# Performance work log

Hardware: AMD Instinct MI355X
Metric: run time of the kernel (lower is better)

## Reference

```python
import jax, jax.numpy as jnp
import numpy as np

B, S, H = 2, 1024, 1024
NH, NKV, HD = 16, 4, 64
E, K, I = 8, 2, 3584
EPS = 1e-5
THETA = 1e6


def setup_inputs() -> dict:
    key = jax.random.key(0)
    ks = jax.random.split(key, 12)
    sc = 0.02
    return {
        "hidden_states": jax.random.normal(ks[0], (B, S, H), jnp.float32),
        "ln1_w": jnp.ones((H,), jnp.float32),
        "wq": jax.random.normal(ks[1], (H, NH * HD), jnp.float32) * sc,
        "wk": jax.random.normal(ks[2], (H, NKV * HD), jnp.float32) * sc,
        "wv": jax.random.normal(ks[3], (H, NKV * HD), jnp.float32) * sc,
        "wo": jax.random.normal(ks[4], (NH * HD, H), jnp.float32) * sc,
        "ln2_w": jnp.ones((H,), jnp.float32),
        "router_w": jax.random.normal(ks[5], (H, E), jnp.float32) * sc,
        "w_gate": jax.random.normal(ks[6], (E, H, I), jnp.float32) * sc,
        "w_up": jax.random.normal(ks[7], (E, H, I), jnp.float32) * sc,
        "w_down": jax.random.normal(ks[8], (E, I, H), jnp.float32) * sc,
    }


def _rmsnorm(x, w):
    xf = x.astype(jnp.float32)
    return (xf * jax.lax.rsqrt(jnp.mean(xf * xf, axis=-1, keepdims=True) + EPS)).astype(x.dtype) * w


def _rope_cos_sin():
    inv_freq = 1.0 / (THETA ** (jnp.arange(0, HD, 2, dtype=jnp.float32) / HD))
    ang = jnp.arange(S, dtype=jnp.float32)[:, None] * inv_freq[None, :]  # [S, HD//2]
    emb = jnp.concatenate([ang, ang], axis=-1)  # [S, HD]
    return jnp.cos(emb)[None, :, None, :], jnp.sin(emb)[None, :, None, :]


def _rotate_half(x):
    return jnp.concatenate([-x[..., HD // 2:], x[..., : HD // 2]], axis=-1)


def _attention(x, wq, wk, wv, wo):
    q = (x @ wq).reshape(B, S, NH, HD)
    k = (x @ wk).reshape(B, S, NKV, HD)
    v = (x @ wv).reshape(B, S, NKV, HD)
    cos, sin = _rope_cos_sin()
    q = q * cos + _rotate_half(q) * sin
    k = k * cos + _rotate_half(k) * sin
    rep = NH // NKV
    k = jnp.repeat(k, rep, axis=2)  # [B,S,NH,HD]
    v = jnp.repeat(v, rep, axis=2)
    scores = jnp.einsum("bqhd,bkhd->bhqk", q, k) / jnp.sqrt(jnp.float32(HD))
    causal = jnp.tril(jnp.ones((S, S), bool))
    scores = jnp.where(causal[None, None], scores, jnp.float32(-1e9))
    probs = jax.nn.softmax(scores, axis=-1)
    out = jnp.einsum("bhqk,bkhd->bqhd", probs, v).reshape(B, S, NH * HD)
    return out @ wo


def _moe(x, router_w, w_gate, w_up, w_down):
    t = x.reshape(B * S, H)  # [T,H]
    logits = t @ router_w  # [T,E]
    probs = jax.nn.softmax(logits.astype(jnp.float32), axis=-1)
    top_v, top_i = jax.lax.top_k(probs, K)
    top_v = top_v / jnp.sum(top_v, axis=-1, keepdims=True)  # normalize_top_k_affinities
    # dense combine weights [T,E]
    dense_w = jnp.sum(jax.nn.one_hot(top_i, E, dtype=t.dtype) * top_v[..., None], axis=1)
    out = jnp.zeros_like(t)
    for e in range(E):  # small fixed expert loop (E=8)
        g = jax.nn.silu(t @ w_gate[e]) * (t @ w_up[e])
        out = out + dense_w[:, e:e + 1] * (g @ w_down[e])
    return out.reshape(B, S, H)


def reference(hidden_states, ln1_w, wq, wk, wv, wo, ln2_w, router_w, w_gate, w_up, w_down):
    residual = hidden_states
    h = _rmsnorm(hidden_states, ln1_w)
    h = residual + _attention(h, wq, wk, wv, wo)
    residual = h
    h2 = _rmsnorm(h, ln2_w)
    h = residual + _moe(h2, router_w, w_gate, w_up, w_down)
    return h
```

## Files before the change

### kernel.cpp

```cpp
#include <hip/hip_runtime.h>
#include <hip/hip_bf16.h>
#include <math.h>

#define B_ 2
#define S_ 1024
#define H_ 1024
#define NH_ 16
#define NKV_ 4
#define HD_ 64
#define E_ 8
#define I_ 3584
#define T_ (B_*S_)

#define BM 64
#define BN 64
#define MBM 128
#define DBM 64
#define MBK 64

typedef __bf16 bf16x8 __attribute__((ext_vector_type(8)));
typedef float f32x4 __attribute__((ext_vector_type(4)));

__device__ __forceinline__ __bf16 bf_hi(float f) { return (__bf16)f; }
__device__ __forceinline__ __bf16 bf_lo(float f, __bf16 h) { return (__bf16)(f - (float)h); }

__device__ __forceinline__ int swz128(int row, int col) {
    return (row * 128 + col * 2) ^ ((row & 7) << 4);
}

__global__ __launch_bounds__(256) void split_bf16_kernel(
    const float* __restrict__ src, __bf16* __restrict__ hi, __bf16* __restrict__ lo,
    float scale, int n8)
{
    int idx = blockIdx.x * 256 + threadIdx.x;
    if (idx >= n8) return;
    const float4* s = (const float4*)src + (size_t)idx * 2;
    float4 a = s[0], b = s[1];
    float f[8] = {a.x, a.y, a.z, a.w, b.x, b.y, b.z, b.w};
    bf16x8 vh, vl;
#pragma unroll
    for (int i = 0; i < 8; i++) {
        float x = f[i] * scale;
        __bf16 h = bf_hi(x);
        vh[i] = h;
        vl[i] = bf_lo(x, h);
    }
    ((bf16x8*)hi)[idx] = vh;
    ((bf16x8*)lo)[idx] = vl;
}

__global__ __launch_bounds__(256) void transpose_cvt_kernel(
    const float* __restrict__ src, __bf16* __restrict__ dst, int M, int N)
{
    int e = blockIdx.z;
    src += (size_t)e * M * N;
    dst += (size_t)e * M * N;
    int n0 = blockIdx.x * 64, m0 = blockIdx.y * 64;
    __shared__ __bf16 Ts[64][72];
    int tid = threadIdx.x;
#pragma unroll
    for (int i = 0; i < 16; i++) {
        int row = i * 4 + (tid >> 6);
        int col = tid & 63;
        Ts[row][col] = (__bf16)src[(size_t)(m0 + row) * N + n0 + col];
    }
    __syncthreads();
#pragma unroll
    for (int j = 0; j < 2; j++) {
        int n = (tid >> 3) + j * 32;
        int k8 = (tid & 7) * 8;
        bf16x8 v;
#pragma unroll
        for (int ii = 0; ii < 8; ii++) v[ii] = Ts[k8 + ii][n];
        *(bf16x8*)(dst + (size_t)(n0 + n) * M + m0 + k8) = v;
    }
}

__global__ __launch_bounds__(256) void rmsnorm_kernel(
    const float* __restrict__ x, const float* __restrict__ w,
    __bf16* __restrict__ outb, float* __restrict__ outf)
{
    int row = blockIdx.x;
    int tid = threadIdx.x;
    const float* xr = x + (size_t)row * H_;
    float vals[4];
    float ss = 0.f;
#pragma unroll
    for (int i = 0; i < 4; i++) {
        vals[i] = xr[tid + 256 * i];
        ss += vals[i] * vals[i];
    }
#pragma unroll
    for (int off = 32; off; off >>= 1) ss += __shfl_xor(ss, off);
    __shared__ float red[4];
    int wid = tid >> 6;
    if ((tid & 63) == 0) red[wid] = ss;
    __syncthreads();
    float tot = red[0] + red[1] + red[2] + red[3];
    float scale = rsqrtf(tot * (1.0f / H_) + 1e-5f);
#pragma unroll
    for (int i = 0; i < 4; i++) {
        float y = vals[i] * scale * w[tid + 256 * i];
        outb[(size_t)row * H_ + tid + 256 * i] = (__bf16)y;
        if (outf) outf[(size_t)row * H_ + tid + 256 * i] = y;
    }
}

__global__ __launch_bounds__(256) void gemm_bf16bt(
    const __bf16* __restrict__ A, const __bf16* __restrict__ BT,
    float* __restrict__ C, const float* __restrict__ res,
    int M, int N, int Kd)
{
    int m0 = blockIdx.y * DBM;
    int n0 = blockIdx.x * BN;
    __shared__ __bf16 As[2][DBM * MBK];
    __shared__ __bf16 Bs[2][BN * MBK];
    int tid = threadIdx.x;
    int lane = tid & 63, wid = tid >> 6;
    f32x4 acc[4] = {};
    int ar = tid >> 2, ac = (tid & 3) * 16;
    int bn = tid >> 2, bc = (tid & 3) * 16;
    const __bf16* abase = A + (size_t)(m0 + ar) * Kd + ac;
    const __bf16* bbase = BT + (size_t)(n0 + bn) * Kd + bc;
    {
        char* Asb = (char*)As[0];
        char* Bsb = (char*)Bs[0];
#pragma unroll
        for (int g = 0; g < 2; g++) {
            *(bf16x8*)(Asb + swz128(ar, ac + g * 8)) = *(const bf16x8*)(abase + g * 8);
            *(bf16x8*)(Bsb + swz128(bn, bc + g * 8)) = *(const bf16x8*)(bbase + g * 8);
        }
    }
    bf16x8 pa[2], pb[2];
    if (Kd > MBK) {
#pragma unroll
        for (int g = 0; g < 2; g++) {
            pa[g] = *(const bf16x8*)(abase + MBK + g * 8);
            pb[g] = *(const bf16x8*)(bbase + MBK + g * 8);
        }
    }
    int cur = 0;
    int r = lane & 15, q8 = (lane >> 4) * 8;
    for (int kt = 0; kt < Kd; kt += MBK) {
        __syncthreads();
        char* Asb = (char*)As[cur];
        char* Bsb = (char*)Bs[cur];
#pragma unroll
        for (int kk = 0; kk < 2; kk++) {
            bf16x8 af = *(const bf16x8*)(Asb + swz128(wid * 16 + r, kk * 32 + q8));
            bf16x8 bfr[4];
#pragma unroll
            for (int n = 0; n < 4; n++)
                bfr[n] = *(const bf16x8*)(Bsb + swz128(n * 16 + r, kk * 32 + q8));
#pragma unroll
            for (int n = 0; n < 4; n++)
                acc[n] = __builtin_amdgcn_mfma_f32_16x16x32_bf16(af, bfr[n], acc[n], 0, 0, 0);
        }
        int kn = kt + MBK;
        if (kn < Kd) {
            char* Asw = (char*)As[cur ^ 1];
            char* Bsw = (char*)Bs[cur ^ 1];
#pragma unroll
            for (int g = 0; g < 2; g++) {
                *(bf16x8*)(Asw + swz128(ar, ac + g * 8)) = pa[g];
                *(bf16x8*)(Bsw + swz128(bn, bc + g * 8)) = pb[g];
            }
            int k2 = kn + MBK;
            if (k2 < Kd) {
#pragma unroll
                for (int g = 0; g < 2; g++) {
                    pa[g] = *(const bf16x8*)(abase + k2 + g * 8);
                    pb[g] = *(const bf16x8*)(bbase + k2 + g * 8);
                }
            }
            cur ^= 1;
        }
    }
    int cl = lane & 15, rb = (lane >> 4) * 4;
#pragma unroll
    for (int n = 0; n < 4; n++)
#pragma unroll
        for (int j = 0; j < 4; j++) {
            int row = m0 + wid * 16 + rb + j;
            int col = n0 + n * 16 + cl;
            size_t o = (size_t)row * N + col;
            float v = acc[n][j];
            if (res) v += res[o];
            C[o] = v;
        }
}

__global__ void rope_split_kernel(
    const float* __restrict__ x, __bf16* __restrict__ hi, __bf16* __restrict__ lo,
    float scale, int heads, int total)
{
    int idx = blockIdx.x * blockDim.x + threadIdx.x;
    if (idx >= total) return;
    int j = idx & 31;
    int th = idx >> 5;
    int h = th % heads;
    int t = th / heads;
    int s = t & (S_ - 1);
    float inv = powf(1e6f, -(float)j / 32.0f);
    float ang = (float)s * inv;
    float c = cosf(ang), sn = sinf(ang);
    size_t base = (size_t)t * heads * HD_ + (size_t)h * HD_;
    float x1 = x[base + j], x2 = x[base + 32 + j];
    float y1 = (x1 * c - x2 * sn) * scale;
    float y2 = (x2 * c + x1 * sn) * scale;
    __bf16 h1 = bf_hi(y1), h2 = bf_hi(y2);
    hi[base + j] = h1;       lo[base + j] = bf_lo(y1, h1);
    hi[base + 32 + j] = h2;  lo[base + 32 + j] = bf_lo(y2, h2);
}

#define LP 72
__global__ __launch_bounds__(256) void flash_kernel(
    const __bf16* __restrict__ qhi, const __bf16* __restrict__ qlo_g,
    const __bf16* __restrict__ khi, const __bf16* __restrict__ klo,
    const __bf16* __restrict__ vhi, const __bf16* __restrict__ vlo,
    __bf16* __restrict__ o)
{
    __shared__ __bf16 Ks [64][LP];
    __shared__ __bf16 Ksl[64][LP];
    __shared__ __bf16 Vt [64][LP];
    __shared__ __bf16 Vtl[64][LP];
    __shared__ __bf16 Pl [4][16][LP];
    __shared__ __bf16 Pll[4][16][LP];

    int tid = threadIdx.x;
    int lane = tid & 63, wid = tid >> 6;
    int qr = lane & 15, quad = lane >> 4;
    int qt = (S_ / 16 - 1) - blockIdx.x;
    int kvh = blockIdx.y, b = blockIdx.z;
    int h = kvh * 4 + wid;
    int s0 = qt * 16;

    size_t qoff = ((size_t)(b * S_ + s0 + qr) * NH_ + h) * HD_ + quad * 8;
    bf16x8 qf[2], qlo[2];
#pragma unroll
    for (int ks = 0; ks < 2; ks++) {
        qf[ks]  = *(const bf16x8*)(qhi  + qoff + ks * 32);
        qlo[ks] = *(const bf16x8*)(qlo_g + qoff + ks * 32);
    }

    float m_run[4], l_run[4];
    f32x4 o_acc[4] = {};
#pragma unroll
    for (int j = 0; j < 4; j++) { m_run[j] = -1e30f; l_run[j] = 0.f; }

    int skey = tid >> 2, shd0 = (tid & 3) * 16;
    int vhd = tid & 63, vkey0 = (tid >> 6) * 16;

    for (int kt = 0; kt <= s0 + 15; kt += 64) {
        __syncthreads();
        {
            size_t koff = ((size_t)(b * S_ + kt + skey) * NKV_ + kvh) * HD_ + shd0;
            *(bf16x8*)&Ks [skey][shd0]     = *(const bf16x8*)(khi + koff);
            *(bf16x8*)&Ks [skey][shd0 + 8] = *(const bf16x8*)(khi + koff + 8);
            *(bf16x8*)&Ksl[skey][shd0]     = *(const bf16x8*)(klo + koff);
            *(bf16x8*)&Ksl[skey][shd0 + 8] = *(const bf16x8*)(klo + koff + 8);
        }
        {
            const __bf16* vh = vhi + ((size_t)(b * S_ + kt + vkey0) * NKV_ + kvh) * HD_ + vhd;
            const __bf16* vl = vlo + ((size_t)(b * S_ + kt + vkey0) * NKV_ + kvh) * HD_ + vhd;
            bf16x8 th0, th1, tl0, tl1;
#pragma unroll
            for (int i = 0; i < 8; i++) {
                th0[i] = vh[(size_t)i * (NKV_ * HD_)];
                th1[i] = vh[(size_t)(i + 8) * (NKV_ * HD_)];
                tl0[i] = vl[(size_t)i * (NKV_ * HD_)];
                tl1[i] = vl[(size_t)(i + 8) * (NKV_ * HD_)];
            }
            *(bf16x8*)&Vt [vhd][vkey0]     = th0;
            *(bf16x8*)&Vt [vhd][vkey0 + 8] = th1;
            *(bf16x8*)&Vtl[vhd][vkey0]     = tl0;
            *(bf16x8*)&Vtl[vhd][vkey0 + 8] = tl1;
        }
        __syncthreads();

        f32x4 sc4[4];
#pragma unroll
        for (int sub = 0; sub < 4; sub++) {
            int krow = sub * 16 + qr;
            bf16x8 kh0 = *(const bf16x8*)&Ks [krow][quad * 8];
            bf16x8 kh1 = *(const bf16x8*)&Ks [krow][32 + quad * 8];
            bf16x8 kl0 = *(const bf16x8*)&Ksl[krow][quad * 8];
            bf16x8 kl1 = *(const bf16x8*)&Ksl[krow][32 + quad * 8];
            f32x4 z = {};
            z = __builtin_amdgcn_mfma_f32_16x16x32_bf16(qf[0],  kh0, z, 0, 0, 0);
            z = __builtin_amdgcn_mfma_f32_16x16x32_bf16(qf[1],  kh1, z, 0, 0, 0);
            z = __builtin_amdgcn_mfma_f32_16x16x32_bf16(qlo[0], kh0, z, 0, 0, 0);
            z = __builtin_amdgcn_mfma_f32_16x16x32_bf16(qlo[1], kh1, z, 0, 0, 0);
            z = __builtin_amdgcn_mfma_f32_16x16x32_bf16(qf[0],  kl0, z, 0, 0, 0);
            z = __builtin_amdgcn_mfma_f32_16x16x32_bf16(qf[1],  kl1, z, 0, 0, 0);
            sc4[sub] = z;
        }
        if (kt + 63 > s0) {
#pragma unroll
            for (int sub = 0; sub < 4; sub++)
#pragma unroll
                for (int j = 0; j < 4; j++) {
                    int key = kt + sub * 16 + qr;
                    int row = s0 + quad * 4 + j;
                    if (key > row) sc4[sub][j] = -1e30f;
                }
        }
#pragma unroll
        for (int j = 0; j < 4; j++) {
            float mx = fmaxf(fmaxf(sc4[0][j], sc4[1][j]), fmaxf(sc4[2][j], sc4[3][j]));
#pragma unroll
            for (int off = 1; off < 16; off <<= 1) mx = fmaxf(mx, __shfl_xor(mx, off));
            float mn = fmaxf(m_run[j], mx);
            float scale = __expf(m_run[j] - mn);
            m_run[j] = mn;
            float rs = 0.f;
#pragma unroll
            for (int sub = 0; sub < 4; sub++) {
                float pe = __expf(sc4[sub][j] - mn);
                sc4[sub][j] = pe;
                rs += pe;
            }
#pragma unroll
            for (int off = 1; off < 16; off <<= 1) rs += __shfl_xor(rs, off);
            l_run[j] = l_run[j] * scale + rs;
#pragma unroll
            for (int sub = 0; sub < 4; sub++) o_acc[sub][j] *= scale;
        }
#pragma unroll
        for (int sub = 0; sub < 4; sub++)
#pragma unroll
            for (int j = 0; j < 4; j++) {
                float pe = sc4[sub][j];
                __bf16 hh = bf_hi(pe);
                Pl [wid][quad * 4 + j][sub * 16 + qr] = hh;
                Pll[wid][quad * 4 + j][sub * 16 + qr] = bf_lo(pe, hh);
            }
        __syncthreads();
        bf16x8 ph0 = *(const bf16x8*)&Pl [wid][qr][quad * 8];
        bf16x8 ph1 = *(const bf16x8*)&Pl [wid][qr][32 + quad * 8];
        bf16x8 pl0 = *(const bf16x8*)&Pll[wid][qr][quad * 8];
        bf16x8 pl1 = *(const bf16x8*)&Pll[wid][qr][32 + quad * 8];
#pragma unroll
        for (int sub = 0; sub < 4; sub++) {
            int vrow = sub * 16 + qr;
            bf16x8 vh0 = *(const bf16x8*)&Vt [vrow][quad * 8];
            bf16x8 vh1 = *(const bf16x8*)&Vt [vrow][32 + quad * 8];
            bf16x8 vl0 = *(const bf16x8*)&Vtl[vrow][quad * 8];
            bf16x8 vl1 = *(const bf16x8*)&Vtl[vrow][32 + quad * 8];
            o_acc[sub] = __builtin_amdgcn_mfma_f32_16x16x32_bf16(ph0, vh0, o_acc[sub], 0, 0, 0);
            o_acc[sub] = __builtin_amdgcn_mfma_f32_16x16x32_bf16(ph1, vh1, o_acc[sub], 0, 0, 0);
            o_acc[sub] = __builtin_amdgcn_mfma_f32_16x16x32_bf16(ph0, vl0, o_acc[sub], 0, 0, 0);
            o_acc[sub] = __builtin_amdgcn_mfma_f32_16x16x32_bf16(ph1, vl1, o_acc[sub], 0, 0, 0);
            o_acc[sub] = __builtin_amdgcn_mfma_f32_16x16x32_bf16(pl0, vh0, o_acc[sub], 0, 0, 0);
            o_acc[sub] = __builtin_amdgcn_mfma_f32_16x16x32_bf16(pl1, vh1, o_acc[sub], 0, 0, 0);
        }
    }
#pragma unroll
    for (int j = 0; j < 4; j++) {
        float inv = 1.f / l_run[j];
        int row = s0 + quad * 4 + j;
#pragma unroll
        for (int sub = 0; sub < 4; sub++)
            o[((size_t)(b * S_ + row) * NH_ + h) * HD_ + sub * 16 + qr] = (__bf16)(o_acc[sub][j] * inv);
    }
}

__global__ __launch_bounds__(256) void router_kernel(
    const float* __restrict__ xn, const float* __restrict__ rw,
    int* __restrict__ top_i, float* __restrict__ top_w)
{
    int wid = threadIdx.x >> 6, lane = threadIdx.x & 63;
    int t = blockIdx.x * 4 + wid;
    const float* xr = xn + (size_t)t * H_;
    float acc[E_] = {};
    for (int c = 0; c < H_ / 64; c++) {
        float xd = xr[c * 64 + lane];
        const float* wrow = rw + (size_t)(c * 64 + lane) * E_;
#pragma unroll
        for (int e = 0; e < E_; e++) acc[e] += xd * wrow[e];
    }
#pragma unroll
    for (int e = 0; e < E_; e++) {
        float r = acc[e];
#pragma unroll
        for (int off = 32; off; off >>= 1) r += __shfl_xor(r, off);
        acc[e] = r;
    }
    if (lane == 0) {
        float mx = acc[0];
        for (int e = 1; e < E_; e++) mx = fmaxf(mx, acc[e]);
        float p[E_], sum = 0.f;
        for (int e = 0; e < E_; e++) { p[e] = __expf(acc[e] - mx); sum += p[e]; }
        float inv_s = 1.f / sum;
        for (int e = 0; e < E_; e++) p[e] *= inv_s;
        int i0 = 0;
        for (int e = 1; e < E_; e++) if (p[e] > p[i0]) i0 = e;
        int i1 = (i0 == 0) ? 1 : 0;
        for (int e = 0; e < E_; e++) if (e != i0 && p[e] > p[i1]) i1 = e;
        float v0 = p[i0], v1 = p[i1], inv = 1.f / (v0 + v1);
        top_i[t * 2] = i0; top_i[t * 2 + 1] = i1;
        top_w[t * 2] = v0 * inv; top_w[t * 2 + 1] = v1 * inv;
    }
}

__global__ void assign_kernel(
    const int* __restrict__ top_i, const float* __restrict__ top_w,
    int* __restrict__ tlist, int* __restrict__ pair_pos,
    int* __restrict__ counts, int* __restrict__ offsets)
{
    __shared__ int cnt[E_], off[E_], fill[E_];
    int tid = threadIdx.x;
    if (tid < E_) { cnt[tid] = 0; fill[tid] = 0; }
    __syncthreads();
    for (int t = tid; t < T_; t += 256) {
        atomicAdd(&cnt[top_i[t * 2]], 1);
        atomicAdd(&cnt[top_i[t * 2 + 1]], 1);
    }
    __syncthreads();
    if (tid == 0) {
        int o = 0;
        for (int e = 0; e < E_; e++) { off[e] = o; o += cnt[e]; }
    }
    __syncthreads();
    for (int t = tid; t < T_; t += 256) {
        for (int j = 0; j < 2; j++) {
            int e = top_i[t * 2 + j];
            int pos = off[e] + atomicAdd(&fill[e], 1);
            tlist[pos] = t;
            pair_pos[t * 2 + j] = pos;
        }
    }
    __syncthreads();
    if (tid < E_) { counts[tid] = cnt[tid]; offsets[tid] = off[tid]; }
}

__global__ __launch_bounds__(256) void moe_gemm_gateup(
    const __bf16* __restrict__ Xb, const __bf16* __restrict__ WgT, const __bf16* __restrict__ WuT,
    __bf16* __restrict__ act, const int* __restrict__ tlist,
    const int* __restrict__ counts, const int* __restrict__ offsets)
{
    int e = blockIdx.z;
    int cnt = counts[e], off = offsets[e];
    int m0 = blockIdx.y * MBM;
    if (m0 >= cnt) return;
    int n0 = blockIdx.x * BN;
    const __bf16* Bg = WgT + (size_t)e * H_ * I_;
    const __bf16* Bu = WuT + (size_t)e * H_ * I_;
    __shared__ __bf16 As[2][MBM * MBK];
    __shared__ __bf16 Gs[2][BN * MBK];
    __shared__ __bf16 Us[2][BN * MBK];
    __shared__ int rowidx[MBM];
    int tid = threadIdx.x;
    if (tid < MBM) {
        int rl = m0 + tid;
        rowidx[tid] = tlist[off + ((rl < cnt) ? rl : 0)];
    }
    __syncthreads();
    int lane = tid & 63, wid = tid >> 6;
    f32x4 accg[2][4] = {}, accu[2][4] = {};
    int ar = tid >> 1, ac = (tid & 1) * 32;
    int bn = tid >> 2, bc = (tid & 3) * 16;
    const __bf16* abase = Xb + (size_t)rowidx[ar] * H_ + ac;
    const __bf16* gbase = Bg + (size_t)(n0 + bn) * H_ + bc;
    const __bf16* ubase = Bu + (size_t)(n0 + bn) * H_ + bc;
    {
        char* Asb = (char*)As[0];
        char* Gsb = (char*)Gs[0];
        char* Usb = (char*)Us[0];
#pragma unroll
        for (int g = 0; g < 4; g++)
            *(bf16x8*)(Asb + swz128(ar, ac + g * 8)) = *(const bf16x8*)(abase + g * 8);
#pragma unroll
        for (int g = 0; g < 2; g++) {
            *(bf16x8*)(Gsb + swz128(bn, bc + g * 8)) = *(const bf16x8*)(gbase + g * 8);
            *(bf16x8*)(Usb + swz128(bn, bc + g * 8)) = *(const bf16x8*)(ubase + g * 8);
        }
    }
    bf16x8 pa[4], pg[2], pu[2];
    if (H_ > MBK) {
#pragma unroll
        for (int g = 0; g < 4; g++) pa[g] = *(const bf16x8*)(abase + MBK + g * 8);
#pragma unroll
        for (int g = 0; g < 2; g++) {
            pg[g] = *(const bf16x8*)(gbase + MBK + g * 8);
            pu[g] = *(const bf16x8*)(ubase + MBK + g * 8);
        }
    }
    int cur = 0;
    int r = lane & 15, q8 = (lane >> 4) * 8;
    for (int kt = 0; kt < H_; kt += MBK) {
        __syncthreads();
        char* Asb = (char*)As[cur];
        char* Gsb = (char*)Gs[cur];
        char* Usb = (char*)Us[cur];
#pragma unroll
        for (int kk = 0; kk < 2; kk++) {
            bf16x8 af[2], gf[4], uf[4];
#pragma unroll
            for (int m = 0; m < 2; m++)
                af[m] = *(const bf16x8*)(Asb + swz128(wid * 32 + m * 16 + r, kk * 32 + q8));
#pragma unroll
            for (int n = 0; n < 4; n++) {
                gf[n] = *(const bf16x8*)(Gsb + swz128(n * 16 + r, kk * 32 + q8));
                uf[n] = *(const bf16x8*)(Usb + swz128(n * 16 + r, kk * 32 + q8));
            }
#pragma unroll
            for (int m = 0; m < 2; m++)
#pragma unroll
                for (int n = 0; n < 4; n++) {
                    accg[m][n] = __builtin_amdgcn_mfma_f32_16x16x32_bf16(af[m], gf[n], accg[m][n], 0, 0, 0);
                    accu[m][n] = __builtin_amdgcn_mfma_f32_16x16x32_bf16(af[m], uf[n], accu[m][n], 0, 0, 0);
                }
        }
        int kn = kt + MBK;
        if (kn < H_) {
            char* Asw = (char*)As[cur ^ 1];
            char* Gsw = (char*)Gs[cur ^ 1];
            char* Usw = (char*)Us[cur ^ 1];
#pragma unroll
            for (int g = 0; g < 4; g++) *(bf16x8*)(Asw + swz128(ar, ac + g * 8)) = pa[g];
#pragma unroll
            for (int g = 0; g < 2; g++) {
                *(bf16x8*)(Gsw + swz128(bn, bc + g * 8)) = pg[g];
                *(bf16x8*)(Usw + swz128(bn, bc + g * 8)) = pu[g];
            }
            int k2 = kn + MBK;
            if (k2 < H_) {
#pragma unroll
                for (int g = 0; g < 4; g++) pa[g] = *(const bf16x8*)(abase + k2 + g * 8);
#pragma unroll
                for (int g = 0; g < 2; g++) {
                    pg[g] = *(const bf16x8*)(gbase + k2 + g * 8);
                    pu[g] = *(const bf16x8*)(ubase + k2 + g * 8);
                }
            }
            cur ^= 1;
        }
    }
    int cl = lane & 15, rb = (lane >> 4) * 4;
#pragma unroll
    for (int m = 0; m < 2; m++)
#pragma unroll
        for (int n = 0; n < 4; n++)
#pragma unroll
            for (int j = 0; j < 4; j++) {
                int rl = m0 + wid * 32 + m * 16 + rb + j;
                if (rl >= cnt) continue;
                int col = n0 + n * 16 + cl;
                float g = accg[m][n][j], u = accu[m][n][j];
                float sig = 1.f / (1.f + __expf(-g));
                act[(size_t)(off + rl) * I_ + col] = (__bf16)(g * sig * u);
            }
}

__global__ __launch_bounds__(256) void moe_gemm_down(
    const __bf16* __restrict__ act, const __bf16* __restrict__ WdT,
    float* __restrict__ dout, const int* __restrict__ counts, const int* __restrict__ offsets)
{
    int e = blockIdx.z;
    int cnt = counts[e], off = offsets[e];
    int m0 = blockIdx.y * DBM;
    if (m0 >= cnt) return;
    int n0 = blockIdx.x * BN;
    const __bf16* Bw = WdT + (size_t)e * I_ * H_;
    __shared__ __bf16 As[2][DBM * MBK];
    __shared__ __bf16 Bs[2][BN * MBK];
    int tid = threadIdx.x;
    int lane = tid & 63, wid = tid >> 6;
    f32x4 acc[4] = {};
    int ar = tid >> 2, ac = (tid & 3) * 16;
    int bn = tid >> 2, bc = (tid & 3) * 16;
    int arow = m0 + ar; if (arow >= cnt) arow = cnt - 1;
    const __bf16* abase = act + (size_t)(off + arow) * I_ + ac;
    const __bf16* bbase = Bw + (size_t)(n0 + bn) * I_ + bc;
    {
        char* Asb = (char*)As[0];
        char* Bsb = (char*)Bs[0];
#pragma unroll
        for (int g = 0; g < 2; g++) {
            *(bf16x8*)(Asb + swz128(ar, ac + g * 8)) = *(const bf16x8*)(abase + g * 8);
            *(bf16x8*)(Bsb + swz128(bn, bc + g * 8)) = *(const bf16x8*)(bbase + g * 8);
        }
    }
    bf16x8 pa[2], pb[2];
    if (I_ > MBK) {
#pragma unroll
        for (int g = 0; g < 2; g++) {
            pa[g] = *(const bf16x8*)(abase + MBK + g * 8);
            pb[g] = *(const bf16x8*)(bbase + MBK + g * 8);
        }
    }
    int cur = 0;
    int r = lane & 15, q8 = (lane >> 4) * 8;
    for (int kt = 0; kt < I_; kt += MBK) {
        __syncthreads();
        char* Asb = (char*)As[cur];
        char* Bsb = (char*)Bs[cur];
#pragma unroll
        for (int kk = 0; kk < 2; kk++) {
            bf16x8 af = *(const bf16x8*)(Asb + swz128(wid * 16 + r, kk * 32 + q8));
            bf16x8 bfr[4];
#pragma unroll
            for (int n = 0; n < 4; n++)
                bfr[n] = *(const bf16x8*)(Bsb + swz128(n * 16 + r, kk * 32 + q8));
#pragma unroll
            for (int n = 0; n < 4; n++)
                acc[n] = __builtin_amdgcn_mfma_f32_16x16x32_bf16(af, bfr[n], acc[n], 0, 0, 0);
        }
        int kn = kt + MBK;
        if (kn < I_) {
            char* Asw = (char*)As[cur ^ 1];
            char* Bsw = (char*)Bs[cur ^ 1];
#pragma unroll
            for (int g = 0; g < 2; g++) {
                *(bf16x8*)(Asw + swz128(ar, ac + g * 8)) = pa[g];
                *(bf16x8*)(Bsw + swz128(bn, bc + g * 8)) = pb[g];
            }
            int k2 = kn + MBK;
            if (k2 < I_) {
#pragma unroll
                for (int g = 0; g < 2; g++) {
                    pa[g] = *(const bf16x8*)(abase + k2 + g * 8);
                    pb[g] = *(const bf16x8*)(bbase + k2 + g * 8);
                }
            }
            cur ^= 1;
        }
    }
    int cl = lane & 15, rb = (lane >> 4) * 4;
#pragma unroll
    for (int n = 0; n < 4; n++)
#pragma unroll
        for (int j = 0; j < 4; j++) {
            int rl = m0 + wid * 16 + rb + j;
            if (rl >= cnt) continue;
            int col = n0 + n * 16 + cl;
            dout[(size_t)(off + rl) * H_ + col] = acc[n][j];
        }
}

__global__ __launch_bounds__(256) void combine_kernel(
    const float* __restrict__ hres, const float* __restrict__ dout,
    const int* __restrict__ pair_pos, const float* __restrict__ top_w,
    float* __restrict__ out)
{
    int idx = blockIdx.x * 256 + threadIdx.x;
    int t = idx >> 10, d = idx & 1023;
    float v = hres[idx];
    int p0 = pair_pos[t * 2], p1 = pair_pos[t * 2 + 1];
    v += top_w[t * 2] * dout[(size_t)p0 * H_ + d]
       + top_w[t * 2 + 1] * dout[(size_t)p1 * H_ + d];
    out[idx] = v;
}

extern "C" void kernel_launch(void* const* d_in, const int* in_sizes, int n_in,
                              void* d_out, int out_size, void* d_ws, size_t ws_size,
                              hipStream_t stream) {
    const float* hidden = (const float*)d_in[0];
    const float* ln1 = (const float*)d_in[1];
    const float* wq = (const float*)d_in[2];
    const float* wk = (const float*)d_in[3];
    const float* wv = (const float*)d_in[4];
    const float* wo = (const float*)d_in[5];
    const float* ln2 = (const float*)d_in[6];
    const float* rw = (const float*)d_in[7];
    const float* wg = (const float*)d_in[8];
    const float* wu = (const float*)d_in[9];
    const float* wd = (const float*)d_in[10];
    float* out = (float*)d_out;

    char* ws = (char*)d_ws;
    size_t o = 0;
    auto alloc = [&](size_t bytes) -> void* {
        void* p = ws + o;
        o += (bytes + 255) & ~(size_t)255;
        return p;
    };
    float* xn   = (float*)alloc((size_t)T_ * H_ * 4);
    float* qb   = (float*)alloc((size_t)T_ * NH_ * HD_ * 4);
    float* kb   = (float*)alloc((size_t)T_ * NKV_ * HD_ * 4);
    float* vb   = (float*)alloc((size_t)T_ * NKV_ * HD_ * 4);
    float* hres = (float*)alloc((size_t)T_ * H_ * 4);
    int*   top_i    = (int*)alloc((size_t)T_ * 2 * 4);
    float* top_w    = (float*)alloc((size_t)T_ * 2 * 4);
    int*   pair_pos = (int*)alloc((size_t)T_ * 2 * 4);
    int*   tlist    = (int*)alloc((size_t)T_ * 2 * 4);
    int*   counts   = (int*)alloc(E_ * 4);
    int*   offsets  = (int*)alloc(E_ * 4);
    __bf16* actb  = (__bf16*)alloc((size_t)T_ * 2 * I_ * 2);
    float*  doutb = (float*)alloc((size_t)T_ * 2 * H_ * 4);
    __bf16* xnb1 = (__bf16*)alloc((size_t)T_ * H_ * 2);
    __bf16* xnb  = (__bf16*)alloc((size_t)T_ * H_ * 2);
    __bf16* attnb = (__bf16*)alloc((size_t)T_ * H_ * 2);
    __bf16* wgt = (__bf16*)alloc((size_t)E_ * H_ * I_ * 2);
    __bf16* wut = (__bf16*)alloc((size_t)E_ * H_ * I_ * 2);
    __bf16* wdt = (__bf16*)alloc((size_t)E_ * I_ * H_ * 2);
    __bf16* wqt = (__bf16*)alloc((size_t)H_ * NH_ * HD_ * 2);
    __bf16* wkt = (__bf16*)alloc((size_t)H_ * NKV_ * HD_ * 2);
    __bf16* wvt = (__bf16*)alloc((size_t)H_ * NKV_ * HD_ * 2);
    __bf16* wot = (__bf16*)alloc((size_t)NH_ * HD_ * H_ * 2);
    __bf16* qhib = (__bf16*)alloc((size_t)T_ * NH_ * HD_ * 2);
    __bf16* qlob = (__bf16*)alloc((size_t)T_ * NH_ * HD_ * 2);
    __bf16* khib = (__bf16*)alloc((size_t)T_ * NKV_ * HD_ * 2);
    __bf16* klob = (__bf16*)alloc((size_t)T_ * NKV_ * HD_ * 2);
    __bf16* vhib = (__bf16*)alloc((size_t)T_ * NKV_ * HD_ * 2);
    __bf16* vlob = (__bf16*)alloc((size_t)T_ * NKV_ * HD_ * 2);

    transpose_cvt_kernel<<<dim3(I_ / 64, H_ / 64, E_), 256, 0, stream>>>(wg, wgt, H_, I_);
    transpose_cvt_kernel<<<dim3(I_ / 64, H_ / 64, E_), 256, 0, stream>>>(wu, wut, H_, I_);
    transpose_cvt_kernel<<<dim3(H_ / 64, I_ / 64, E_), 256, 0, stream>>>(wd, wdt, I_, H_);
    transpose_cvt_kernel<<<dim3((NH_ * HD_) / 64, H_ / 64, 1), 256, 0, stream>>>(wq, wqt, H_, NH_ * HD_);
    transpose_cvt_kernel<<<dim3((NKV_ * HD_) / 64, H_ / 64, 1), 256, 0, stream>>>(wk, wkt, H_, NKV_ * HD_);
    transpose_cvt_kernel<<<dim3((NKV_ * HD_) / 64, H_ / 64, 1), 256, 0, stream>>>(wv, wvt, H_, NKV_ * HD_);
    transpose_cvt_kernel<<<dim3(H_ / 64, (NH_ * HD_) / 64, 1), 256, 0, stream>>>(wo, wot, NH_ * HD_, H_);

    rmsnorm_kernel<<<T_, 256, 0, stream>>>(hidden, ln1, xnb1, nullptr);
    gemm_bf16bt<<<dim3((NH_ * HD_) / BN, T_ / DBM), 256, 0, stream>>>(xnb1, wqt, qb, nullptr, T_, NH_ * HD_, H_);
    gemm_bf16bt<<<dim3((NKV_ * HD_) / BN, T_ / DBM), 256, 0, stream>>>(xnb1, wkt, kb, nullptr, T_, NKV_ * HD_, H_);
    gemm_bf16bt<<<dim3((NKV_ * HD_) / BN, T_ / DBM), 256, 0, stream>>>(xnb1, wvt, vb, nullptr, T_, NKV_ * HD_, H_);
    {
        int tq = T_ * NH_ * 32, tk = T_ * NKV_ * 32;
        rope_split_kernel<<<(tq + 255) / 256, 256, 0, stream>>>(qb, qhib, qlob, 0.125f, NH_, tq);
        rope_split_kernel<<<(tk + 255) / 256, 256, 0, stream>>>(kb, khib, klob, 1.0f, NKV_, tk);
        int nk8 = T_ * NKV_ * HD_ / 8;
        split_bf16_kernel<<<(nk8 + 255) / 256, 256, 0, stream>>>(vb, vhib, vlob, 1.0f, nk8);
    }
    flash_kernel<<<dim3(S_ / 16, NKV_, B_), 256, 0, stream>>>(qhib, qlob, khib, klob, vhib, vlob, attnb);
    gemm_bf16bt<<<dim3(H_ / BN, T_ / DBM), 256, 0, stream>>>(attnb, wot, hres, hidden, T_, H_, NH_ * HD_);
    rmsnorm_kernel<<<T_, 256, 0, stream>>>(hres, ln2, xnb, xn);
    router_kernel<<<T_ / 4, 256, 0, stream>>>(xn, rw, top_i, top_w);
    assign_kernel<<<1, 256, 0, stream>>>(top_i, top_w, tlist, pair_pos, counts, offsets);
    moe_gemm_gateup<<<dim3(I_ / BN, T_ / MBM, E_), 256, 0, stream>>>(xnb, wgt, wut, actb, tlist, counts, offsets);
    moe_gemm_down<<<dim3(H_ / BN, T_ / DBM, E_), 256, 0, stream>>>(actb, wdt, doutb, counts, offsets);
    combine_kernel<<<(T_ * H_) / 256, 256, 0, stream>>>(hres, doutb, pair_pos, top_w, out);
}
```

Measured before the change: 431.7 us.

## Use direct global-to-LDS loads in MoE GEMMs with single-buffered K=32 tiles

Result: slower. 441.7 us (+2.3%).

```diff
diff --git a/kernel.cpp b/kernel.cpp
--- a/kernel.cpp
+++ b/kernel.cpp
@@ -17,6 +17,7 @@
 #define MBM 128
 #define DBM 64
 #define MBK 64
+#define KST 32
 
 typedef __bf16 bf16x8 __attribute__((ext_vector_type(8)));
 typedef float f32x4 __attribute__((ext_vector_type(4)));
@@ -26,6 +27,12 @@
 
 __device__ __forceinline__ int swz128(int row, int col) {
     return (row * 128 + col * 2) ^ ((row & 7) << 4);
+}
+
+__device__ __forceinline__ void gload16(const __bf16* g, __bf16* l) {
+    __builtin_amdgcn_global_load_lds(
+        (const __attribute__((address_space(1))) void*)g,
+        (__attribute__((address_space(3))) void*)l, 16, 0, 0);
 }
 
 __global__ __launch_bounds__(256) void split_bf16_kernel(
@@ -446,9 +453,9 @@
     int n0 = blockIdx.x * BN;
     const __bf16* Bg = WgT + (size_t)e * H_ * I_;
     const __bf16* Bu = WuT + (size_t)e * H_ * I_;
-    __shared__ __bf16 As[2][MBM * MBK];
-    __shared__ __bf16 Gs[2][BN * MBK];
-    __shared__ __bf16 Us[2][BN * MBK];
+    __shared__ __bf16 As[MBM * KST];
+    __shared__ __bf16 Gs[BN * KST];
+    __shared__ __bf16 Us[BN * KST];
     __shared__ int rowidx[MBM];
     int tid = threadIdx.x;
     if (tid < MBM) {
@@ -457,85 +464,43 @@
     }
     __syncthreads();
     int lane = tid & 63, wid = tid >> 6;
+    const __bf16* a_src[2];
+#pragma unroll
+    for (int i = 0; i < 2; i++) {
+        int chunk = (wid * 2 + i) * 64 + lane;
+        a_src[i] = Xb + (size_t)rowidx[chunk >> 2] * H_ + (chunk & 3) * 8;
+    }
+    int bchunk = wid * 64 + lane;
+    const __bf16* g_src = Bg + (size_t)(n0 + (bchunk >> 2)) * H_ + (bchunk & 3) * 8;
+    const __bf16* u_src = Bu + (size_t)(n0 + (bchunk >> 2)) * H_ + (bchunk & 3) * 8;
     f32x4 accg[2][4] = {}, accu[2][4] = {};
-    int ar = tid >> 1, ac = (tid & 1) * 32;
-    int bn = tid >> 2, bc = (tid & 3) * 16;
-    const __bf16* abase = Xb + (size_t)rowidx[ar] * H_ + ac;
-    const __bf16* gbase = Bg + (size_t)(n0 + bn) * H_ + bc;
-    const __bf16* ubase = Bu + (size_t)(n0 + bn) * H_ + bc;
-    {
-        char* Asb = (char*)As[0];
-        char* Gsb = (char*)Gs[0];
-        char* Usb = (char*)Us[0];
-#pragma unroll
-        for (int g = 0; g < 4; g++)
-            *(bf16x8*)(Asb + swz128(ar, ac + g * 8)) = *(const bf16x8*)(abase + g * 8);
-#pragma unroll
-        for (int g = 0; g < 2; g++) {
-            *(bf16x8*)(Gsb + swz128(bn, bc + g * 8)) = *(const bf16x8*)(gbase + g * 8);
-            *(bf16x8*)(Usb + swz128(bn, bc + g * 8)) = *(const bf16x8*)(ubase + g * 8);
-        }
-    }
-    bf16x8 pa[4], pg[2], pu[2];
-    if (H_ > MBK) {
-#pragma unroll
-        for (int g = 0; g < 4; g++) pa[g] = *(const bf16x8*)(abase + MBK + g * 8);
-#pragma unroll
-        for (int g = 0; g < 2; g++) {
-            pg[g] = *(const bf16x8*)(gbase + MBK + g * 8);
-            pu[g] = *(const bf16x8*)(ubase + MBK + g * 8);
-        }
-    }
-    int cur = 0;
     int r = lane & 15, q8 = (lane >> 4) * 8;
-    for (int kt = 0; kt < H_; kt += MBK) {
-        __syncthreads();
-        char* Asb = (char*)As[cur];
-        char* Gsb = (char*)Gs[cur];
-        char* Usb = (char*)Us[cur];
-#pragma unroll
-        for (int kk = 0; kk < 2; kk++) {
-            bf16x8 af[2], gf[4], uf[4];
-#pragma unroll
-            for (int m = 0; m < 2; m++)
-                af[m] = *(const bf16x8*)(Asb + swz128(wid * 32 + m * 16 + r, kk * 32 + q8));
+    char* Asb = (char*)As;
+    char* Gsb = (char*)Gs;
+    char* Usb = (char*)Us;
+    for (int kt = 0; kt < H_; kt += KST) {
+        gload16(a_src[0] + kt, As + (wid * 2 + 0) * 512);
+        gload16(a_src[1] + kt, As + (wid * 2 + 1) * 512);
+        gload16(g_src + kt, Gs + wid * 512);
+        gload16(u_src + kt, Us + wid * 512);
+        __syncthreads();
+        bf16x8 af[2], gf[4], uf[4];
+#pragma unroll
+        for (int m = 0; m < 2; m++)
+            af[m] = *(const bf16x8*)(Asb + (wid * 32 + m * 16 + r) * 64 + q8 * 2);
+#pragma unroll
+        for (int n = 0; n < 4; n++) {
+            gf[n] = *(const bf16x8*)(Gsb + (n * 16 + r) * 64 + q8 * 2);
+            uf[n] = *(const bf16x8*)(Usb + (n * 16 + r) * 64 + q8 * 2);
+        }
+#pragma unroll
+        for (int m = 0; m < 2; m++)
 #pragma unroll
             for (int n = 0; n < 4; n++) {
-                gf[n] = *(const bf16x8*)(Gsb + swz128(n * 16 + r, kk * 32 + q8));
-                uf[n] = *(const bf16x8*)(Usb + swz128(n * 16 + r, kk * 32 + q8));
+                accg[m][n] = __builtin_amdgcn_mfma_f32_16x16x32_bf16(af[m], gf[n], accg[m][n], 0, 0, 0);
+                accu[m][n] = __builtin_amdgcn_mfma_f32_16x16x32_bf16(af[m], uf[n], accu[m][n], 0, 0, 0);
             }
-#pragma unroll
-            for (int m = 0; m < 2; m++)
-#pragma unroll
-                for (int n = 0; n < 4; n++) {
-                    accg[m][n] = __builtin_amdgcn_mfma_f32_16x16x32_bf16(af[m], gf[n], accg[m][n], 0, 0, 0);
-                    accu[m][n] = __builtin_amdgcn_mfma_f32_16x16x32_bf16(af[m], uf[n], accu[m][n], 0, 0, 0);
-                }
-        }
-        int kn = kt + MBK;
-        if (kn < H_) {
-            char* Asw = (char*)As[cur ^ 1];
-            char* Gsw = (char*)Gs[cur ^ 1];
-            char* Usw = (char*)Us[cur ^ 1];
-#pragma unroll
-            for (int g = 0; g < 4; g++) *(bf16x8*)(Asw + swz128(ar, ac + g * 8)) = pa[g];
-#pragma unroll
-            for (int g = 0; g < 2; g++) {
-                *(bf16x8*)(Gsw + swz128(bn, bc + g * 8)) = pg[g];
-                *(bf16x8*)(Usw + swz128(bn, bc + g * 8)) = pu[g];
-            }
-            int k2 = kn + MBK;
-            if (k2 < H_) {
-#pragma unroll
-                for (int g = 0; g < 4; g++) pa[g] = *(const bf16x8*)(abase + k2 + g * 8);
-#pragma unroll
-                for (int g = 0; g < 2; g++) {
-                    pg[g] = *(const bf16x8*)(gbase + k2 + g * 8);
-                    pu[g] = *(const bf16x8*)(ubase + k2 + g * 8);
-                }
-            }
-            cur ^= 1;
-        }
+        __syncthreads();
     }
     int cl = lane & 15, rb = (lane >> 4) * 4;
 #pragma unroll
@@ -563,69 +528,32 @@
     if (m0 >= cnt) return;
     int n0 = blockIdx.x * BN;
     const __bf16* Bw = WdT + (size_t)e * I_ * H_;
-    __shared__ __bf16 As[2][DBM * MBK];
-    __shared__ __bf16 Bs[2][BN * MBK];
+    __shared__ __bf16 As[DBM * KST];
+    __shared__ __bf16 Bs[BN * KST];
     int tid = threadIdx.x;
     int lane = tid & 63, wid = tid >> 6;
+    int chunk = wid * 64 + lane;
+    int crow = chunk >> 2, ccg = chunk & 3;
+    int arow = m0 + crow; if (arow >= cnt) arow = cnt - 1;
+    const __bf16* a_src = act + (size_t)(off + arow) * I_ + ccg * 8;
+    const __bf16* b_src = Bw + (size_t)(n0 + crow) * I_ + ccg * 8;
     f32x4 acc[4] = {};
-    int ar = tid >> 2, ac = (tid & 3) * 16;
-    int bn = tid >> 2, bc = (tid & 3) * 16;
-    int arow = m0 + ar; if (arow >= cnt) arow = cnt - 1;
-    const __bf16* abase = act + (size_t)(off + arow) * I_ + ac;
-    const __bf16* bbase = Bw + (size_t)(n0 + bn) * I_ + bc;
-    {
-        char* Asb = (char*)As[0];
-        char* Bsb = (char*)Bs[0];
-#pragma unroll
-        for (int g = 0; g < 2; g++) {
-            *(bf16x8*)(Asb + swz128(ar, ac + g * 8)) = *(const bf16x8*)(abase + g * 8);
-            *(bf16x8*)(Bsb + swz128(bn, bc + g * 8)) = *(const bf16x8*)(bbase + g * 8);
-        }
-    }
-    bf16x8 pa[2], pb[2];
-    if (I_ > MBK) {
-#pragma unroll
-        for (int g = 0; g < 2; g++) {
-            pa[g] = *(const bf16x8*)(abase + MBK + g * 8);
-            pb[g] = *(const bf16x8*)(bbase + MBK + g * 8);
-        }
-    }
-    int cur = 0;
     int r = lane & 15, q8 = (lane >> 4) * 8;
-    for (int kt = 0; kt < I_; kt += MBK) {
-        __syncthreads();
-        char* Asb = (char*)As[cur];
-        char* Bsb = (char*)Bs[cur];
-#pragma unroll
-        for (int kk = 0; kk < 2; kk++) {
-            bf16x8 af = *(const bf16x8*)(Asb + swz128(wid * 16 + r, kk * 32 + q8));
-            bf16x8 bfr[4];
-#pragma unroll
-            for (int n = 0; n < 4; n++)
-                bfr[n] = *(const bf16x8*)(Bsb + swz128(n * 16 + r, kk * 32 + q8));
-#pragma unroll
-            for (int n = 0; n < 4; n++)
-                acc[n] = __builtin_amdgcn_mfma_f32_16x16x32_bf16(af, bfr[n], acc[n], 0, 0, 0);
-        }
-        int kn = kt + MBK;
-        if (kn < I_) {
-            char* Asw = (char*)As[cur ^ 1];
-            char* Bsw = (char*)Bs[cur ^ 1];
-#pragma unroll
-            for (int g = 0; g < 2; g++) {
-                *(bf16x8*)(Asw + swz128(ar, ac + g * 8)) = pa[g];
-                *(bf16x8*)(Bsw + swz128(bn, bc + g * 8)) = pb[g];
-            }
-            int k2 = kn + MBK;
-            if (k2 < I_) {
-#pragma unroll
-                for (int g = 0; g < 2; g++) {
-                    pa[g] = *(const bf16x8*)(abase + k2 + g * 8);
-                    pb[g] = *(const bf16x8*)(bbase + k2 + g * 8);
-                }
-            }
-            cur ^= 1;
-        }
+    char* Asb = (char*)As;
+    char* Bsb = (char*)Bs;
+    for (int kt = 0; kt < I_; kt += KST) {
+        gload16(a_src + kt, As + wid * 512);
+        gload16(b_src + kt, Bs + wid * 512);
+        __syncthreads();
+        bf16x8 af = *(const bf16x8*)(Asb + (wid * 16 + r) * 64 + q8 * 2);
+        bf16x8 bfr[4];
+#pragma unroll
+        for (int n = 0; n < 4; n++)
+            bfr[n] = *(const bf16x8*)(Bsb + (n * 16 + r) * 64 + q8 * 2);
+#pragma unroll
+        for (int n = 0; n < 4; n++)
+            acc[n] = __builtin_amdgcn_mfma_f32_16x16x32_bf16(af, bfr[n], acc[n], 0, 0, 0);
+        __syncthreads();
     }
     int cl = lane & 15, rb = (lane >> 4) * 4;
 #pragma unroll
```
